# Kernel tuning notes

Hardware: AMD Instinct MI355X
Metric: run time of the kernel (lower is better)

The kernel has to match this reference:

```python
import jax, jax.numpy as jnp
import numpy as np

L, E, H, R = 6, 1024, 8, 33
DH = E // H
FF = 4 * E
B, S = 8, 512


def _layer_norm(x, g, b, eps=1e-5):
    m = jnp.mean(x, axis=-1, keepdims=True)
    v = jnp.mean(jnp.square(x - m), axis=-1, keepdims=True)
    return (x - m) * jax.lax.rsqrt(v + eps) * g + b


def setup_inputs() -> dict:
    key = jax.random.key(0)
    ks = jax.random.split(key, 24)
    rn = lambda k, shape, s=0.02: (jax.random.normal(k, shape, jnp.float32) * s)
    inp = {
        'enc_padded': jax.random.normal(ks[0], (B, S, E), jnp.float32),
        'relations': jax.random.randint(ks[1], (B, S, S), 0, R),
        'enc_lengths': jax.random.randint(ks[2], (B,), 1, S + 1),
        'Wq': rn(ks[3], (L, E, E)), 'bq': jnp.zeros((L, E), jnp.float32),
        'Wk': rn(ks[4], (L, E, E)), 'bk': jnp.zeros((L, E), jnp.float32),
        'Wv': rn(ks[5], (L, E, E)), 'bv': jnp.zeros((L, E), jnp.float32),
        'Wo': rn(ks[6], (L, E, E)), 'bo': jnp.zeros((L, E), jnp.float32),
        'rel_k': rn(ks[7], (L, R, DH)),
        'rel_v': rn(ks[8], (L, R, DH)),
        'W1': rn(ks[9], (L, E, FF)), 'b1': jnp.zeros((L, FF), jnp.float32),
        'W2': rn(ks[10], (L, FF, E)), 'b2': jnp.zeros((L, E), jnp.float32),
        'ln1_g': jnp.ones((L, E), jnp.float32), 'ln1_b': jnp.zeros((L, E), jnp.float32),
        'ln2_g': jnp.ones((L, E), jnp.float32), 'ln2_b': jnp.zeros((L, E), jnp.float32),
        'lnf_g': jnp.ones((E,), jnp.float32), 'lnf_b': jnp.zeros((E,), jnp.float32),
    }
    return inp


def reference(enc_padded, relations, enc_lengths, Wq, bq, Wk, bk, Wv, bv, Wo, bo,
              rel_k, rel_v, W1, b1, W2, b2, ln1_g, ln1_b, ln2_g, ln2_b, lnf_g, lnf_b):
    x = enc_padded  # [B,S,E]
    dt = x.dtype
    # attention mask: valid iff both query and key positions are within seq length
    pos = jnp.arange(S)
    valid = pos[None, :] < enc_lengths[:, None]            # [B,S]
    mask2d = valid[:, :, None] & valid[:, None, :]          # [B,S,S]
    # one-hot relation indicator, shared across layers (R=33 is small)
    rel_oh = jax.nn.one_hot(relations, R, dtype=dt)        # [B,S,S,R]
    scale = 1.0 / np.sqrt(DH).astype(np.float32)

    def split_heads(t):  # [B,S,E] -> [B,H,S,DH]
        return t.reshape(B, S, H, DH).transpose(0, 2, 1, 3)

    for l in range(L):
        # --- relation-aware self-attention (pre-LN sublayer) ---
        h = _layer_norm(x, ln1_g[l], ln1_b[l])
        q = split_heads(h @ Wq[l] + bq[l])
        k = split_heads(h @ Wk[l] + bk[l])
        v = split_heads(h @ Wv[l] + bv[l])
        scores = jnp.einsum('bhid,bhjd->bhij', q, k)
        # relation key bias: q_i . rel_k[rel[i,j]]  via small [B,H,S,R] GEMM + one-hot contraction
        qr = jnp.einsum('bhid,rd->bhir', q, rel_k[l])
        scores = (scores + jnp.einsum('bhir,bijr->bhij', qr, rel_oh)) * scale
        scores = jnp.where(mask2d[:, None], scores, jnp.asarray(-1e9, dt))
        attn = jax.nn.softmax(scores, axis=-1)              # [B,H,S,S]
        out = jnp.einsum('bhij,bhjd->bhid', attn, v)
        # relation value bias: sum_j attn_ij * rel_v[rel[i,j]]
        a_rel = jnp.einsum('bhij,bijr->bhir', attn, rel_oh)
        out = out + jnp.einsum('bhir,rd->bhid', a_rel, rel_v[l])
        out = out.transpose(0, 2, 1, 3).reshape(B, S, E) @ Wo[l] + bo[l]
        x = x + out
        # --- position-wise feed-forward (pre-LN sublayer) ---
        h2 = _layer_norm(x, ln2_g[l], ln2_b[l])
        x = x + (jax.nn.relu(h2 @ W1[l] + b1[l]) @ W2[l] + b2[l])
    return _layer_norm(x, lnf_g, lnf_b)
```

## Files before the change

kernel.cpp:

```cpp
#include <hip/hip_runtime.h>

#define LNUM 6
#define EDIM 1024
#define HNUM 8
#define DHD  128
#define RNUM 33
#define FFD  4096
#define BNUM 8
#define SLEN 512
#define TOK  (BNUM*SLEN)

typedef __attribute__((ext_vector_type(8))) short bf16x8;
typedef __attribute__((ext_vector_type(4))) float f32x4;
typedef unsigned short u16;
typedef unsigned int u32;

__device__ __forceinline__ u16 f2b(float f) {
  u32 u = __builtin_bit_cast(u32, f);
  u32 r = u + 0x7FFFu + ((u >> 16) & 1u);
  return (u16)(r >> 16);
}
__device__ __forceinline__ u32 pck(float a, float b) { return (u32)f2b(a) | ((u32)f2b(b) << 16); }

#define GL16(gp, lp) __builtin_amdgcn_global_load_lds(                        \
    (const __attribute__((address_space(1))) void*)(gp),                      \
    (__attribute__((address_space(3))) void*)(lp), 16, 0, 0)

#define WAITVM16 do { asm volatile("s_waitcnt vmcnt(16)" ::: "memory"); \
                      __builtin_amdgcn_sched_barrier(0); } while (0)
#define WAITVM8 do { asm volatile("s_waitcnt vmcnt(8)" ::: "memory"); \
                     __builtin_amdgcn_sched_barrier(0); } while (0)
#define WAITVM4 do { asm volatile("s_waitcnt vmcnt(4)" ::: "memory"); \
                     __builtin_amdgcn_sched_barrier(0); } while (0)
#define WAITVM0 do { asm volatile("s_waitcnt vmcnt(0)" ::: "memory"); \
                     __builtin_amdgcn_sched_barrier(0); } while (0)

template<int BF16OUT>
__global__ __launch_bounds__(256) void ln_kernel(const float* __restrict__ x,
                                                 const float* __restrict__ g,
                                                 const float* __restrict__ be,
                                                 void* __restrict__ o) {
  int row = blockIdx.x;
  int t = threadIdx.x;
  const float* xr = x + (size_t)row * EDIM;
  float4 xv = *reinterpret_cast<const float4*>(xr + t * 4);
  float s1 = xv.x + xv.y + xv.z + xv.w;
  float s2 = xv.x*xv.x + xv.y*xv.y + xv.z*xv.z + xv.w*xv.w;
#pragma unroll
  for (int off = 32; off >= 1; off >>= 1) {
    s1 += __shfl_down(s1, off, 64);
    s2 += __shfl_down(s2, off, 64);
  }
  __shared__ float r1[4], r2[4];
  if ((t & 63) == 0) { r1[t >> 6] = s1; r2[t >> 6] = s2; }
  __syncthreads();
  s1 = r1[0] + r1[1] + r1[2] + r1[3];
  s2 = r2[0] + r2[1] + r2[2] + r2[3];
  float mean = s1 * (1.0f / EDIM);
  float var  = s2 * (1.0f / EDIM) - mean * mean;
  float rstd = rsqrtf(var + 1e-5f);
  float4 gv = *reinterpret_cast<const float4*>(g + t * 4);
  float4 bv = *reinterpret_cast<const float4*>(be + t * 4);
  float o0 = (xv.x - mean) * rstd * gv.x + bv.x;
  float o1 = (xv.y - mean) * rstd * gv.y + bv.y;
  float o2 = (xv.z - mean) * rstd * gv.z + bv.z;
  float o3 = (xv.w - mean) * rstd * gv.w + bv.w;
  if (BF16OUT) {
    ushort4 ov; ov.x = f2b(o0); ov.y = f2b(o1); ov.z = f2b(o2); ov.w = f2b(o3);
    *reinterpret_cast<ushort4*>((u16*)o + (size_t)row * EDIM + t * 4) = ov;
  } else {
    *reinterpret_cast<float4*>((float*)o + (size_t)row * EDIM + t * 4) = make_float4(o0, o1, o2, o3);
  }
}

__global__ __launch_bounds__(256) void wtrans(const float* __restrict__ src0,
                                              u16* __restrict__ dst0,
                                              int Kd, int Nd, size_t sstride, size_t dstride) {
  __shared__ float Ts[32][33];
  const float* src = src0 + blockIdx.z * sstride;
  u16* dst = dst0 + blockIdx.z * dstride;
  int r0 = blockIdx.y * 32, c0 = blockIdx.x * 32;
  int ty = threadIdx.x >> 3, tx = threadIdx.x & 7;
  float4 v = *reinterpret_cast<const float4*>(src + (size_t)(r0 + ty) * Nd + c0 + tx * 4);
  Ts[ty][tx*4+0] = v.x; Ts[ty][tx*4+1] = v.y; Ts[ty][tx*4+2] = v.z; Ts[ty][tx*4+3] = v.w;
  __syncthreads();
  ushort4 o;
  o.x = f2b(Ts[tx*4+0][ty]); o.y = f2b(Ts[tx*4+1][ty]);
  o.z = f2b(Ts[tx*4+2][ty]); o.w = f2b(Ts[tx*4+3][ty]);
  *reinterpret_cast<ushort4*>(dst + (size_t)(c0 + ty) * Kd + r0 + tx * 4) = o;
}

__global__ __launch_bounds__(256) void relpack(const int* __restrict__ rel,
                                               unsigned char* __restrict__ out) {
  __shared__ int Ts[32][33];
  int bz = blockIdx.z;
  int r0 = blockIdx.y * 32, c0 = blockIdx.x * 32;
  int ty = threadIdx.x >> 3, tx = threadIdx.x & 7;
  const int* src = rel + (size_t)bz * SLEN * SLEN;
  int4 v = *reinterpret_cast<const int4*>(src + (size_t)(r0 + ty) * SLEN + c0 + tx * 4);
  Ts[ty][tx*4+0] = v.x; Ts[ty][tx*4+1] = v.y; Ts[ty][tx*4+2] = v.z; Ts[ty][tx*4+3] = v.w;
  __syncthreads();
  u32 o = (u32)(Ts[tx*4+0][ty] & 255) | ((u32)(Ts[tx*4+1][ty] & 255) << 8) |
          ((u32)(Ts[tx*4+2][ty] & 255) << 16) | ((u32)(Ts[tx*4+3][ty] & 255) << 24);
  *reinterpret_cast<u32*>(out + (size_t)bz * SLEN * SLEN + (size_t)(c0 + ty) * SLEN + r0 + tx * 4) = o;
}

template<int DEPTH, int BIASMODE, int ACT, int RES, int OUTBF16>
__global__ __launch_bounds__(256) void gemm_bt(const u16* __restrict__ A,
                                               const u16* __restrict__ B,
                                               const float* __restrict__ bias0,
                                               const float* __restrict__ bias1,
                                               const float* __restrict__ res,
                                               void* __restrict__ Cv,
                                               int M, int N, int K) {
  __shared__ u16 As[DEPTH][128 * 64];
  __shared__ u16 Bs[DEPTH][128 * 64];
  int t = threadIdx.x;
  int l = t & 63, w = t >> 6;
  int wm = w & 1, wn = w >> 1;
  int m0 = blockIdx.y * 128, n0 = blockIdx.x * 128;
  f32x4 acc[4][4] = {};
  const u16* Agp = A + (size_t)(m0 + w * 32 + (l >> 3)) * K + (l & 7) * 8;
  const u16* Bgp = B + (size_t)(n0 + w * 32 + (l >> 3)) * K + (l & 7) * 8;
  const int nst = K >> 6;
  auto issue = [&](int k0, int bi) {
#pragma unroll
    for (int u = 0; u < 4; ++u) {
      GL16(Agp + (size_t)(u * 8) * K + k0, &As[bi][w * 2048 + u * 512]);
      GL16(Bgp + (size_t)(u * 8) * K + k0, &Bs[bi][w * 2048 + u * 512]);
    }
  };
  issue(0, 0);
  if (DEPTH == 3 && nst > 1) issue(64, 1);
  for (int i = 0; i < nst; ++i) {
    int cur = (DEPTH == 3) ? (i % 3) : (i & 1);
    if (DEPTH == 3) {
      if (i + 2 < nst)      { issue((i + 2) * 64, (i + 2) % 3); WAITVM16; }
      else if (i + 1 < nst) { WAITVM8; }
      else                  { WAITVM0; }
    } else {
      if (i + 1 < nst) { issue((i + 1) * 64, cur ^ 1); WAITVM8; }
      else             { WAITVM0; }
    }
    __builtin_amdgcn_s_barrier();
    const u16* Asc = As[cur];
    const u16* Bsc = Bs[cur];
#pragma unroll
    for (int d4 = 0; d4 < 2; ++d4) {
      bf16x8 af[4];
#pragma unroll
      for (int fm = 0; fm < 4; ++fm) {
        int row = wm * 64 + fm * 16 + (l & 15);
        af[fm] = *reinterpret_cast<const bf16x8*>(Asc + row * 64 + (d4 * 4 + (l >> 4)) * 8);
      }
#pragma unroll
      for (int fn = 0; fn < 4; ++fn) {
        int row = wn * 64 + fn * 16 + (l & 15);
        bf16x8 bf = *reinterpret_cast<const bf16x8*>(Bsc + row * 64 + (d4 * 4 + (l >> 4)) * 8);
#pragma unroll
        for (int fm = 0; fm < 4; ++fm)
          acc[fm][fn] = __builtin_amdgcn_mfma_f32_16x16x32_bf16(af[fm], bf, acc[fm][fn], 0, 0, 0);
      }
    }
    __builtin_amdgcn_s_barrier();
  }
#pragma unroll
  for (int fm = 0; fm < 4; ++fm)
#pragma unroll
    for (int fn = 0; fn < 4; ++fn)
#pragma unroll
      for (int e = 0; e < 4; ++e) {
        int m = m0 + wm * 64 + fm * 16 + (l >> 4) * 4 + e;
        int n = n0 + wn * 64 + fn * 16 + (l & 15);
        float v = acc[fm][fn][e];
        if (BIASMODE == 0) v += bias0[n];
        if (BIASMODE == 1) v += bias0[m];
        if (BIASMODE == 2) v += (n < 1024) ? bias0[n] : bias1[n - 1024];
        if (ACT == 1) v = fmaxf(v, 0.f);
        if (RES == 1) v += res[(size_t)m * N + n];
        if (OUTBF16) ((u16*)Cv)[(size_t)m * N + n] = f2b(v);
        else ((float*)Cv)[(size_t)m * N + n] = v;
      }
}

#define A_P  0
#define A_Q  16384
#define A_PS 32768
#define A_QR 40960
#define A_AR 50176
#define A_LS 59392
#define A_SM 59648

__global__ __launch_bounds__(256, 2) void attn_kernel(const u16* __restrict__ qk,
                                                      const u16* __restrict__ vt,
                                                      const unsigned char* __restrict__ rel8,
                                                      const int* __restrict__ lens,
                                                      const float* __restrict__ relk,
                                                      const float* __restrict__ relv,
                                                      u16* __restrict__ outb) {
  __align__(16) __shared__ char sm[A_SM];
  char*  Pb  = sm + A_P;
  char*  Qb  = sm + A_Q;
  char*  PSb = sm + A_PS;
  float* QR  = (float*)(sm + A_QR);
  float* AREL = (float*)(sm + A_AR);
  float* LSUM = (float*)(sm + A_LS);

  const int t = threadIdx.x;
  const int l = t & 63, w = t >> 6;
  const int lg = l >> 4;
  const int ll = l & 15;
  const int bx = blockIdx.x;
  const int xcd = bx & 7, rem = bx >> 3, slot = rem & 7, it = rem >> 3;
  const int g = slot * 8 + xcd;
  const int b = g >> 3, hh = g & 7;
  const int i0 = it * 64;
  const int len = lens[b];
  const float scale = 0.08838834764831845f;
  char* PSw = PSb + w * 2048;

  auto issueK = [&](int kt) {
#pragma unroll
    for (int u = 0; u < 4; ++u) {
      int row = w * 16 + u * 4 + (lg);
      int sb = (ll * 16) ^ (((u * 4 + lg) & 7) << 4);
      const u16* gp = qk + (size_t)(b * SLEN + kt * 64 + row) * 2048 + 1024 + hh * DHD + (sb >> 1);
      GL16(gp, Pb + (w * 4 + u) * 1024);
    }
  };
  auto issueV = [&](int kt) {
#pragma unroll
    for (int u = 0; u < 4; ++u) {
      int row = w * 32 + u * 8 + (l >> 3);
      int sb = ((l & 7) * 16) ^ ((l >> 3) << 4);
      const u16* gp = vt + (size_t)(hh * DHD + row) * TOK + b * SLEN + kt * 64 + (sb >> 1);
      GL16(gp, Qb + (w * 4 + u) * 1024);
    }
  };

  u32 relw[4];
  const unsigned char* relbase = rel8 + (size_t)b * SLEN * SLEN + (i0 + w * 16 + lg * 4);
  {
    const unsigned char* rb = relbase + (size_t)ll * SLEN;
#pragma unroll
    for (int fj = 0; fj < 4; ++fj)
      relw[fj] = *reinterpret_cast<const u32*>(rb + (size_t)(fj * 16) * SLEN);
  }
  for (int idx = l; idx < 16 * 36; idx += 64) AREL[w * 16 * 36 + idx] = 0.f;
  if (t < 192) {
    int r = t >> 2, sub = t & 3;
#pragma unroll
    for (int u = 0; u < 4; ++u) {
      int seg = sub * 4 + u;
      uint4 o;
      if (r < RNUM) {
        float4 f0 = *reinterpret_cast<const float4*>(relk + r * DHD + seg * 8);
        float4 f1 = *reinterpret_cast<const float4*>(relk + r * DHD + seg * 8 + 4);
        o.x = pck(f0.x, f0.y); o.y = pck(f0.z, f0.w);
        o.z = pck(f1.x, f1.y); o.w = pck(f1.z, f1.w);
      } else { o.x = o.y = o.z = o.w = 0u; }
      *reinterpret_cast<uint4*>(Pb + r * 256 + ((seg * 16) ^ ((r & 7) << 4))) = o;
    }
  }
  bf16x8 aq[4];
  {
    const u16* qrow = qk + (size_t)(b * SLEN + i0 + w * 16 + ll) * 2048 + hh * DHD;
#pragma unroll
    for (int d4 = 0; d4 < 4; ++d4)
      aq[d4] = *reinterpret_cast<const bf16x8*>(qrow + (d4 * 4 + lg) * 8);
  }
  __syncthreads();
#pragma unroll
  for (int rb = 0; rb < 3; ++rb) {
    f32x4 acc = {};
#pragma unroll
    for (int d4 = 0; d4 < 4; ++d4) {
      int rr = rb * 16 + ll;
      bf16x8 br = *reinterpret_cast<const bf16x8*>(Pb + rr * 256 + (((d4 * 4 + lg) * 16) ^ ((rr & 7) << 4)));
      acc = __builtin_amdgcn_mfma_f32_16x16x32_bf16(aq[d4], br, acc, 0, 0, 0);
    }
    int col = rb * 16 + ll;
    if (col < 36)
#pragma unroll
      for (int e = 0; e < 4; ++e)
        QR[(w * 16 + lg * 4 + e) * 36 + col] = acc[e];
  }
  __syncthreads();
  issueK(0);

  bool rowv[4];
#pragma unroll
  for (int e = 0; e < 4; ++e) rowv[e] = (i0 + w * 16 + lg * 4 + e) < len;

  float m_[4];
#pragma unroll
  for (int e = 0; e < 4; ++e) m_[e] = -3.0e38f;
  f32x4 oacc[8] = {};

  for (int kt = 0; kt < 8; ++kt) {
    issueV(kt);
    WAITVM4;
    __builtin_amdgcn_s_barrier();
    __builtin_amdgcn_s_setprio(1);
    f32x4 sacc[4];
#pragma unroll
    for (int fj = 0; fj < 4; ++fj) {
      f32x4 a = {};
#pragma unroll
      for (int d4 = 0; d4 < 4; ++d4) {
        int row = fj * 16 + ll;
        bf16x8 bk_ = *reinterpret_cast<const bf16x8*>(Pb + row * 256 + (((d4 * 4 + lg) * 16) ^ ((row & 7) << 4)));
        a = __builtin_amdgcn_mfma_f32_16x16x32_bf16(aq[d4], bk_, a, 0, 0, 0);
      }
      sacc[fj] = a;
    }
    __builtin_amdgcn_s_setprio(0);
#pragma unroll
    for (int fj = 0; fj < 4; ++fj) {
      bool colv = (kt * 64 + fj * 16 + ll) < len;
      u32 rw = relw[fj];
#pragma unroll
      for (int e = 0; e < 4; ++e) {
        int r = (rw >> (8 * e)) & 255;
        float s = (sacc[fj][e] + QR[(w * 16 + lg * 4 + e) * 36 + r]) * scale;
        s = (rowv[e] && colv) ? s : -1e9f;
        sacc[fj][e] = s;
      }
    }
    float pl[4];
#pragma unroll
    for (int e = 0; e < 4; ++e)
      pl[e] = fmaxf(fmaxf(sacc[0][e], sacc[1][e]), fmaxf(sacc[2][e], sacc[3][e]));
    bool ok = (pl[0] <= m_[0] + 8.f) && (pl[1] <= m_[1] + 8.f) &&
              (pl[2] <= m_[2] + 8.f) && (pl[3] <= m_[3] + 8.f);
    if (!__all(ok)) {
#pragma unroll
      for (int e = 0; e < 4; ++e) {
        float px = pl[e];
        px = fmaxf(px, __shfl_xor(px, 1, 64));
        px = fmaxf(px, __shfl_xor(px, 2, 64));
        px = fmaxf(px, __shfl_xor(px, 4, 64));
        px = fmaxf(px, __shfl_xor(px, 8, 64));
        float mn = fmaxf(m_[e], px);
        float f = __expf(m_[e] - mn);
        m_[e] = mn;
#pragma unroll
        for (int fd = 0; fd < 8; ++fd) oacc[fd][e] *= f;
        if (f != 1.0f) {
          int row = w * 16 + lg * 4 + e;
          AREL[row * 36 + ll] *= f;
          AREL[row * 36 + 16 + ll] *= f;
          if (ll == 0) AREL[row * 36 + 32] *= f;
        }
      }
    }
#pragma unroll
    for (int fj = 0; fj < 4; ++fj) {
      u32 rw = relw[fj];
#pragma unroll
      for (int e = 0; e < 4; ++e) {
        float p = __expf(sacc[fj][e] - m_[e]);
        int iloc = lg * 4 + e;
        atomicAdd(&AREL[(w * 16 + iloc) * 36 + ((rw >> (8 * e)) & 255)], p);
        *reinterpret_cast<u16*>(PSw + iloc * 128 + (((fj * 16 + ll) * 2) ^ ((iloc & 7) << 4))) = f2b(p);
      }
    }
    if (kt < 7) {
      const unsigned char* rb = relbase + (size_t)((kt + 1) * 64 + ll) * SLEN;
#pragma unroll
      for (int fj = 0; fj < 4; ++fj)
        relw[fj] = *reinterpret_cast<const u32*>(rb + (size_t)(fj * 16) * SLEN);
    }
    __builtin_amdgcn_s_barrier();
    if (kt < 7) issueK(kt + 1);
    if (kt < 7) { WAITVM4; } else { WAITVM0; }
    __builtin_amdgcn_s_barrier();
    __builtin_amdgcn_s_setprio(1);
#pragma unroll
    for (int kc = 0; kc < 2; ++kc) {
      bf16x8 pa = *reinterpret_cast<const bf16x8*>(PSw + ll * 128 + (((kc * 4 + lg) * 16) ^ ((ll & 7) << 4)));
#pragma unroll
      for (int fd = 0; fd < 8; ++fd) {
        int row = fd * 16 + ll;
        bf16x8 vb = *reinterpret_cast<const bf16x8*>(Qb + row * 128 + (((kc * 4 + lg) * 16) ^ ((row & 7) << 4)));
        oacc[fd] = __builtin_amdgcn_mfma_f32_16x16x32_bf16(pa, vb, oacc[fd], 0, 0, 0);
      }
    }
    __builtin_amdgcn_s_setprio(0);
    __builtin_amdgcn_s_barrier();
  }
  if (l < 16) {
    int row = w * 16 + l;
    float s = 0.f;
    for (int r = 0; r < RNUM; ++r) s += AREL[row * 36 + r];
    LSUM[row] = s;
  }
#pragma unroll
  for (int e = 0; e < 4; ++e) {
    float inv = 1.0f / LSUM[w * 16 + lg * 4 + e];
#pragma unroll
    for (int fd = 0; fd < 8; ++fd) oacc[fd][e] *= inv;
  }
  for (int idx = t; idx < 128 * 64; idx += 256) {
    int d = idx >> 6, r = idx & 63;
    u16 v = (r < RNUM) ? f2b(relv[r * DHD + d]) : (u16)0;
    *reinterpret_cast<u16*>(Pb + d * 128 + ((r * 2) ^ ((d & 7) << 4))) = v;
  }
  for (int idx = l; idx < 1024; idx += 64) {
    int ri = idx >> 6, r = idx & 63;
    int row = w * 16 + ri;
    float v = (r < RNUM) ? AREL[row * 36 + r] * (1.0f / LSUM[row]) : 0.f;
    *reinterpret_cast<u16*>(PSw + ri * 128 + ((r * 2) ^ ((ri & 7) << 4))) = f2b(v);
  }
  __syncthreads();
#pragma unroll
  for (int kc = 0; kc < 2; ++kc) {
    bf16x8 pa = *reinterpret_cast<const bf16x8*>(PSw + ll * 128 + (((kc * 4 + lg) * 16) ^ ((ll & 7) << 4)));
#pragma unroll
    for (int fd = 0; fd < 8; ++fd) {
      int row = fd * 16 + ll;
      bf16x8 vb = *reinterpret_cast<const bf16x8*>(Pb + row * 128 + (((kc * 4 + lg) * 16) ^ ((row & 7) << 4)));
      oacc[fd] = __builtin_amdgcn_mfma_f32_16x16x32_bf16(pa, vb, oacc[fd], 0, 0, 0);
    }
  }
  char* OSw = Qb + w * 4096;
#pragma unroll
  for (int fd = 0; fd < 8; ++fd)
#pragma unroll
    for (int e = 0; e < 4; ++e)
      *reinterpret_cast<u16*>(OSw + ((lg * 4 + e) * 128 + fd * 16 + ll) * 2) = f2b(oacc[fd][e]);
  __syncthreads();
  {
    int ri = l >> 2, q4 = l & 3;
    const char* srcb = OSw + ri * 256 + q4 * 64;
    u16* dst = outb + (size_t)(b * SLEN + i0 + w * 16 + ri) * EDIM + hh * DHD + q4 * 32;
    uint4 x0 = *reinterpret_cast<const uint4*>(srcb);
    uint4 x1 = *reinterpret_cast<const uint4*>(srcb + 16);
    uint4 x2 = *reinterpret_cast<const uint4*>(srcb + 32);
    uint4 x3 = *reinterpret_cast<const uint4*>(srcb + 48);
    *reinterpret_cast<uint4*>(dst)      = x0;
    *reinterpret_cast<uint4*>(dst + 8)  = x1;
    *reinterpret_cast<uint4*>(dst + 16) = x2;
    *reinterpret_cast<uint4*>(dst + 24) = x3;
  }
}

extern "C" void kernel_launch(void* const* d_in, const int* in_sizes, int n_in,
                              void* d_out, int out_size, void* d_ws, size_t ws_size,
                              hipStream_t stream) {
  const float* enc  = (const float*)d_in[0];
  const int*   rel  = (const int*)d_in[1];
  const int*   lens = (const int*)d_in[2];
  const float* Wq = (const float*)d_in[3];
  const float* bq = (const float*)d_in[4];
  const float* Wk = (const float*)d_in[5];
  const float* bk = (const float*)d_in[6];
  const float* Wv = (const float*)d_in[7];
  const float* bv = (const float*)d_in[8];
  const float* Wo = (const float*)d_in[9];
  const float* bo = (const float*)d_in[10];
  const float* relk = (const float*)d_in[11];
  const float* relv = (const float*)d_in[12];
  const float* W1 = (const float*)d_in[13];
  const float* b1 = (const float*)d_in[14];
  const float* W2 = (const float*)d_in[15];
  const float* b2 = (const float*)d_in[16];
  const float* ln1g = (const float*)d_in[17];
  const float* ln1b = (const float*)d_in[18];
  const float* ln2g = (const float*)d_in[19];
  const float* ln2b = (const float*)d_in[20];
  const float* lnfg = (const float*)d_in[21];
  const float* lnfb = (const float*)d_in[22];
  float* out = (float*)d_out;

  char* W = (char*)d_ws;
  u16* h     = (u16*)W;
  unsigned char* rel8_h = (unsigned char*)W;
  char* U    = W + 8388608;
  u16* qkb   = (u16*)U;
  u16* vtb   = (u16*)(U + 16777216);
  u16* attno = (u16*)(U + 25165824);
  u16* mid   = (u16*)U;
  bool xin = ws_size >= (size_t)83886080;
  float* x = xin ? (float*)(W + 41943040) : out;
  size_t wt_off = xin ? 58720256 : 41943040;
  char* WT = W + wt_off;
  bool big = ws_size >= (size_t)209715200;

  const size_t EE = (size_t)EDIM * EDIM;
  const size_t EF = (size_t)EDIM * FFD;
  size_t wt_bytes = (big ? 6 : 1) * (size_t)(2*EE + EE + EE + EF + EF) * 2;
  bool rel_ded = ws_size >= wt_off + wt_bytes + (size_t)BNUM * SLEN * SLEN + 256;
  unsigned char* rel8 = rel_ded ? (unsigned char*)(WT + wt_bytes) : rel8_h;

  u16 *WqkT, *WvT, *WoT, *W1T, *W2T;
  dim3 blk(256);
  if (big) {
    u16* wqk_all = (u16*)WT;
    u16* wv_all  = wqk_all + 6 * 2 * EE;
    u16* wo_all  = wv_all + 6 * EE;
    u16* w1_all  = wo_all + 6 * EE;
    u16* w2_all  = w1_all + 6 * EF;
    wtrans<<<dim3(32, 32, 6), blk, 0, stream>>>(Wq, wqk_all, 1024, 1024, EE, 2 * EE);
    wtrans<<<dim3(32, 32, 6), blk, 0, stream>>>(Wk, wqk_all + EE, 1024, 1024, EE, 2 * EE);
    wtrans<<<dim3(32, 32, 6), blk, 0, stream>>>(Wv, wv_all, 1024, 1024, EE, EE);
    wtrans<<<dim3(32, 32, 6), blk, 0, stream>>>(Wo, wo_all, 1024, 1024, EE, EE);
    wtrans<<<dim3(128, 32, 6), blk, 0, stream>>>(W1, w1_all, 1024, 4096, EF, EF);
    wtrans<<<dim3(32, 128, 6), blk, 0, stream>>>(W2, w2_all, 4096, 1024, EF, EF);
    WqkT = wqk_all; WvT = wv_all; WoT = wo_all; W1T = w1_all; W2T = w2_all;
  } else {
    WqkT = (u16*)WT;
    WvT  = WqkT + 2 * EE;
    WoT  = WvT + EE;
    W1T  = WoT + EE;
    W2T  = W1T + EF;
  }
  if (rel_ded) relpack<<<dim3(16, 16, 8), blk, 0, stream>>>(rel, rel8);

  dim3 gLN(TOK);
  for (int ll = 0; ll < LNUM; ++ll) {
    u16 *wqkT, *wvT, *woT, *w1T, *w2T;
    if (big) {
      wqkT = WqkT + (size_t)ll * 2 * EE; wvT = WvT + (size_t)ll * EE; woT = WoT + (size_t)ll * EE;
      w1T = W1T + (size_t)ll * EF; w2T = W2T + (size_t)ll * EF;
    } else {
      wqkT = WqkT; wvT = WvT; woT = WoT; w1T = W1T; w2T = W2T;
      wtrans<<<dim3(32, 32, 1), blk, 0, stream>>>(Wq + ll * EE, wqkT, 1024, 1024, 0, 0);
      wtrans<<<dim3(32, 32, 1), blk, 0, stream>>>(Wk + ll * EE, wqkT + EE, 1024, 1024, 0, 0);
      wtrans<<<dim3(32, 32, 1), blk, 0, stream>>>(Wv + ll * EE, wvT, 1024, 1024, 0, 0);
      wtrans<<<dim3(32, 32, 1), blk, 0, stream>>>(Wo + ll * EE, woT, 1024, 1024, 0, 0);
      wtrans<<<dim3(128, 32, 1), blk, 0, stream>>>(W1 + ll * EF, w1T, 1024, 4096, 0, 0);
      wtrans<<<dim3(32, 128, 1), blk, 0, stream>>>(W2 + ll * EF, w2T, 4096, 1024, 0, 0);
    }
    const float* xin_p = (ll == 0) ? enc : x;
    ln_kernel<1><<<gLN, blk, 0, stream>>>(xin_p, ln1g + ll * EDIM, ln1b + ll * EDIM, h);
    gemm_bt<2, 2, 0, 0, 1><<<dim3(16, 32), blk, 0, stream>>>(h, wqkT, bq + ll * EDIM, bk + ll * EDIM,
                                                             nullptr, qkb, TOK, 2048, EDIM);
    gemm_bt<3, 1, 0, 0, 1><<<dim3(32, 8), blk, 0, stream>>>(wvT, h, bv + ll * EDIM, nullptr,
                                                            nullptr, vtb, EDIM, TOK, EDIM);
    if (!rel_ded) relpack<<<dim3(16, 16, 8), blk, 0, stream>>>(rel, rel8);
    attn_kernel<<<dim3(512), blk, 0, stream>>>(qkb, vtb, rel8, lens,
                                               relk + (size_t)ll * RNUM * DHD,
                                               relv + (size_t)ll * RNUM * DHD, attno);
    gemm_bt<3, 0, 0, 1, 0><<<dim3(8, 32), blk, 0, stream>>>(attno, woT, bo + ll * EDIM, nullptr,
                                                            xin_p, x, TOK, EDIM, EDIM);
    ln_kernel<1><<<gLN, blk, 0, stream>>>(x, ln2g + ll * EDIM, ln2b + ll * EDIM, h);
    gemm_bt<2, 0, 1, 0, 1><<<dim3(32, 32), blk, 0, stream>>>(h, w1T, b1 + ll * FFD, nullptr,
                                                             nullptr, mid, TOK, FFD, EDIM);
    gemm_bt<3, 0, 0, 1, 0><<<dim3(8, 32), blk, 0, stream>>>(mid, w2T, b2 + ll * EDIM, nullptr,
                                                            x, x, TOK, EDIM, FFD);
  }
  ln_kernel<0><<<gLN, blk, 0, stream>>>(x, lnfg, lnfb, out);
}
```

Baseline: 2.190 ms.

## Add 256x256-tile GEMM for FFN up-projection and pad attention P buffer

```diff
diff --git a/kernel.cpp b/kernel.cpp
--- a/kernel.cpp
+++ b/kernel.cpp
@@ -183,13 +183,81 @@
       }
 }
 
+template<int BIASMODE, int ACT, int RES, int OUTBF16>
+__global__ __launch_bounds__(512, 2) void gemm_big(const u16* __restrict__ A,
+                                                   const u16* __restrict__ B,
+                                                   const float* __restrict__ bias0,
+                                                   const float* __restrict__ res,
+                                                   void* __restrict__ Cv,
+                                                   int M, int N, int K) {
+  __shared__ u16 As[2][256 * 64];
+  __shared__ u16 Bs[2][256 * 64];
+  int t = threadIdx.x;
+  int l = t & 63, w = t >> 6;
+  int wm = w >> 2, wn = w & 3;
+  int m0 = blockIdx.y * 256, n0 = blockIdx.x * 256;
+  f32x4 acc[8][4] = {};
+  const u16* Agp = A + (size_t)(m0 + w * 32 + (l >> 3)) * K + (l & 7) * 8;
+  const u16* Bgp = B + (size_t)(n0 + w * 32 + (l >> 3)) * K + (l & 7) * 8;
+  const int nst = K >> 6;
+  auto issue = [&](int k0, int bi) {
+#pragma unroll
+    for (int u = 0; u < 4; ++u) {
+      GL16(Agp + (size_t)(u * 8) * K + k0, &As[bi][w * 2048 + u * 512]);
+      GL16(Bgp + (size_t)(u * 8) * K + k0, &Bs[bi][w * 2048 + u * 512]);
+    }
+  };
+  issue(0, 0);
+  for (int i = 0; i < nst; ++i) {
+    int cur = i & 1;
+    if (i + 1 < nst) { issue((i + 1) * 64, cur ^ 1); WAITVM8; }
+    else             { WAITVM0; }
+    __builtin_amdgcn_s_barrier();
+    const u16* Asc = As[cur];
+    const u16* Bsc = Bs[cur];
+#pragma unroll
+    for (int d4 = 0; d4 < 2; ++d4) {
+      bf16x8 bf[4];
+#pragma unroll
+      for (int fn = 0; fn < 4; ++fn) {
+        int row = wn * 64 + fn * 16 + (l & 15);
+        bf[fn] = *reinterpret_cast<const bf16x8*>(Bsc + row * 64 + (d4 * 4 + (l >> 4)) * 8);
+      }
+#pragma unroll
+      for (int fm = 0; fm < 8; ++fm) {
+        int row = wm * 128 + fm * 16 + (l & 15);
+        bf16x8 af = *reinterpret_cast<const bf16x8*>(Asc + row * 64 + (d4 * 4 + (l >> 4)) * 8);
+#pragma unroll
+        for (int fn = 0; fn < 4; ++fn)
+          acc[fm][fn] = __builtin_amdgcn_mfma_f32_16x16x32_bf16(af, bf[fn], acc[fm][fn], 0, 0, 0);
+      }
+    }
+    __builtin_amdgcn_s_barrier();
+  }
+#pragma unroll
+  for (int fm = 0; fm < 8; ++fm)
+#pragma unroll
+    for (int fn = 0; fn < 4; ++fn)
+#pragma unroll
+      for (int e = 0; e < 4; ++e) {
+        int m = m0 + wm * 128 + fm * 16 + (l >> 4) * 4 + e;
+        int n = n0 + wn * 64 + fn * 16 + (l & 15);
+        float v = acc[fm][fn][e];
+        if (BIASMODE == 0) v += bias0[n];
+        if (ACT == 1) v = fmaxf(v, 0.f);
+        if (RES == 1) v += res[(size_t)m * N + n];
+        if (OUTBF16) ((u16*)Cv)[(size_t)m * N + n] = f2b(v);
+        else ((float*)Cv)[(size_t)m * N + n] = v;
+      }
+}
+
 #define A_P  0
 #define A_Q  16384
 #define A_PS 32768
-#define A_QR 40960
-#define A_AR 50176
-#define A_LS 59392
-#define A_SM 59648
+#define A_QR 43008
+#define A_AR 52224
+#define A_LS 61440
+#define A_SM 61696
 
 __global__ __launch_bounds__(256, 2) void attn_kernel(const u16* __restrict__ qk,
                                                       const u16* __restrict__ vt,
@@ -217,7 +285,7 @@
   const int i0 = it * 64;
   const int len = lens[b];
   const float scale = 0.08838834764831845f;
-  char* PSw = PSb + w * 2048;
+  char* PSw = PSb + w * 2560;
 
   auto issueK = [&](int kt) {
 #pragma unroll
@@ -362,7 +430,7 @@
         float p = __expf(sacc[fj][e] - m_[e]);
         int iloc = lg * 4 + e;
         atomicAdd(&AREL[(w * 16 + iloc) * 36 + ((rw >> (8 * e)) & 255)], p);
-        *reinterpret_cast<u16*>(PSw + iloc * 128 + (((fj * 16 + ll) * 2) ^ ((iloc & 7) << 4))) = f2b(p);
+        *reinterpret_cast<u16*>(PSw + iloc * 136 + (fj * 16 + ll) * 2) = f2b(p);
       }
     }
     if (kt < 7) {
@@ -373,12 +441,12 @@
     }
     __builtin_amdgcn_s_barrier();
     if (kt < 7) issueK(kt + 1);
-    if (kt < 7) { WAITVM4; } else { WAITVM0; }
+    if (kt < 7) { WAITVM8; } else { WAITVM0; }
     __builtin_amdgcn_s_barrier();
     __builtin_amdgcn_s_setprio(1);
 #pragma unroll
     for (int kc = 0; kc < 2; ++kc) {
-      bf16x8 pa = *reinterpret_cast<const bf16x8*>(PSw + ll * 128 + (((kc * 4 + lg) * 16) ^ ((ll & 7) << 4)));
+      bf16x8 pa = *reinterpret_cast<const bf16x8*>(PSw + ll * 136 + (kc * 4 + lg) * 16);
 #pragma unroll
       for (int fd = 0; fd < 8; ++fd) {
         int row = fd * 16 + ll;
@@ -545,8 +613,8 @@
     gemm_bt<3, 0, 0, 1, 0><<<dim3(8, 32), blk, 0, stream>>>(attno, woT, bo + ll * EDIM, nullptr,
                                                             xin_p, x, TOK, EDIM, EDIM);
     ln_kernel<1><<<gLN, blk, 0, stream>>>(x, ln2g + ll * EDIM, ln2b + ll * EDIM, h);
-    gemm_bt<2, 0, 1, 0, 1><<<dim3(32, 32), blk, 0, stream>>>(h, w1T, b1 + ll * FFD, nullptr,
-                                                             nullptr, mid, TOK, FFD, EDIM);
+    gemm_big<0, 1, 0, 1><<<dim3(FFD / 256, TOK / 256), dim3(512), 0, stream>>>(
+        h, w1T, b1 + ll * FFD, nullptr, mid, TOK, FFD, EDIM);
     gemm_bt<3, 0, 0, 1, 0><<<dim3(8, 32), blk, 0, stream>>>(mid, w2T, b2 + ll * EDIM, nullptr,
                                                             x, x, TOK, EDIM, FFD);
   }
```

After: 2.168 ms. About the same (-1.0%).
